# Optimization experiments

Measured on AMD Instinct MI355X. Metric: run time of the kernel, lower is better.

The kernel has to match this reference:

```python
import jax, jax.numpy as jnp
import numpy as np

VOCAB, DIM, B, S = 32000, 1024, 64, 512

def setup_inputs() -> dict:
    key = jax.random.key(0)
    ks = jax.random.split(key, 16)
    std = 1.0 / np.sqrt(DIM)
    return {
        "x": jax.random.randint(ks[0], (B,), 0, VOCAB),
        "h": jax.random.normal(ks[1], (B, DIM), jnp.float32),
        "c": jax.random.normal(ks[2], (B, DIM), jnp.float32),
        "enc_y": jax.random.normal(ks[3], (B, S, DIM), jnp.float32),
        "F_emb": jax.random.normal(ks[4], (VOCAB, DIM), jnp.float32),
        "W1_w": jax.random.uniform(ks[5], (DIM, DIM), jnp.float32, -std, std),
        "W1_b": jnp.zeros((DIM,), jnp.float32),
        "W2_w": jax.random.uniform(ks[6], (DIM, DIM), jnp.float32, -std, std),
        "W2_b": jnp.zeros((DIM,), jnp.float32),
        "V_w": jax.random.uniform(ks[7], (1, DIM), jnp.float32, -std, std),
        "V_b": jnp.zeros((1,), jnp.float32),
        "W_ih": jax.random.uniform(ks[8], (4 * DIM, DIM), jnp.float32, -std, std),
        "W_hh": jax.random.uniform(ks[9], (4 * DIM, DIM), jnp.float32, -std, std),
        "b_ih": jax.random.uniform(ks[10], (4 * DIM,), jnp.float32, -std, std),
        "b_hh": jax.random.uniform(ks[11], (4 * DIM,), jnp.float32, -std, std),
        "fc_w": jax.random.uniform(ks[12], (VOCAB, DIM), jnp.float32, -std, std),
        "fc_b": jnp.zeros((VOCAB,), jnp.float32),
    }

def reference(x, h, c, enc_y, F_emb, W1_w, W1_b, W2_w, W2_b, V_w, V_b,
              W_ih, W_hh, b_ih, b_hh, fc_w, fc_b):
    # Bahdanau additive attention (weights returned; context is dead code for layer=1)
    i_s = jnp.einsum('bsd,ed->bse', enc_y, W1_w) + W1_b          # [B,S,D]
    j_s = (h @ W2_w.T + W2_b)[:, None, :]                        # [B,1,D]
    score = jnp.tanh(i_s + j_s)                                  # [B,S,D]
    att = jax.nn.softmax(score @ V_w.T + V_b, axis=1)            # [B,S,1]
    # embedding lookup for the step token
    emb = F_emb[x]                                               # [B,D]
    # single-step LSTM (pytorch gate order: i, f, g, o)
    gates = emb @ W_ih.T + b_ih + h @ W_hh.T + b_hh              # [B,4D]
    ig, fg, gg, og = jnp.split(gates, 4, axis=-1)
    c_new = jax.nn.sigmoid(fg) * c + jax.nn.sigmoid(ig) * jnp.tanh(gg)
    h_new = jax.nn.sigmoid(og) * jnp.tanh(c_new)
    out = h_new + emb                                            # residual skip
    logits = out @ fc_w.T + fc_b                                 # [B,VOCAB]
    return logits, h_new, c_new, att
```

## Files before the change

kernel.cpp:

```cpp
#include <hip/hip_runtime.h>

#define DEV __device__ __forceinline__

typedef __bf16 bf16_t;
typedef bf16_t bf16x8 __attribute__((ext_vector_type(8)));
typedef float f32x4 __attribute__((ext_vector_type(4)));

static constexpr int VOCAB = 32000, DIM = 1024, BATCH = 64, SEQ = 512;
static constexpr int M_SC = BATCH * SEQ;

DEV unsigned short f2bf(float f) {
  unsigned u = __builtin_bit_cast(unsigned, f);
  u += 0x7FFFu + ((u >> 16) & 1u);
  return (unsigned short)(u >> 16);
}

DEV float sigmf(float x) {
  x = fminf(fmaxf(x, -30.f), 30.f);
  return 1.0f / (1.0f + __expf(-x));
}

DEV float tanh_fast(float x) {
  x = fminf(fmaxf(x, -20.f), 20.f);
  float e = __expf(2.0f * x);
  return (e - 1.0f) / (e + 1.0f);
}

DEV void gload_lds16(const void* g, void* l) {
  __builtin_amdgcn_global_load_lds(
      (__attribute__((address_space(1))) void*)(g),
      (__attribute__((address_space(3))) void*)(l), 16, 0, 0);
}

__global__ void __launch_bounds__(256) k_prep(const float* __restrict__ enc,
                                              const float* __restrict__ w1,
                                              unsigned short* __restrict__ enc_b,
                                              unsigned short* __restrict__ w1_b,
                                              float* __restrict__ att_l) {
  int gid = blockIdx.x * 256 + threadIdx.x;
  if (gid < M_SC) att_l[gid] = 0.f;
  const int ENC4 = (M_SC * DIM) / 4;
  const int TOT4 = ENC4 + (DIM * DIM) / 4;
  int stride = gridDim.x * 256;
  for (int i = gid; i < TOT4; i += stride) {
    float4 v;
    unsigned short* dst;
    if (i < ENC4) {
      v = ((const float4*)enc)[i];
      dst = enc_b + (size_t)i * 4;
    } else {
      v = ((const float4*)w1)[i - ENC4];
      dst = w1_b + (size_t)(i - ENC4) * 4;
    }
    ushort4 o;
    o.x = f2bf(v.x); o.y = f2bf(v.y); o.z = f2bf(v.z); o.w = f2bf(v.w);
    *(ushort4*)dst = o;
  }
}

__global__ void k_embed(const int* __restrict__ x, const float* __restrict__ Femb,
                        const float* __restrict__ h, float* __restrict__ emb_f,
                        unsigned short* __restrict__ eh_b, unsigned short* __restrict__ h_b) {
  int b = blockIdx.x;
  int tok = x[b];
  for (int d = threadIdx.x; d < DIM; d += blockDim.x) {
    float e = Femb[(size_t)tok * DIM + d];
    float hv = h[b * DIM + d];
    emb_f[b * DIM + d] = e;
    unsigned short eb = f2bf(e), hb = f2bf(hv);
    eh_b[b * 2 * DIM + d] = eb;
    eh_b[b * 2 * DIM + DIM + d] = hb;
    h_b[b * DIM + d] = hb;
  }
}

__global__ void __launch_bounds__(256) k_skinny(
    const unsigned short* __restrict__ A, int lda,
    const float* __restrict__ B1, const float* __restrict__ B2, int ksplit,
    const float* __restrict__ bias, float* __restrict__ C, int N, int K) {
  __shared__ unsigned short As[64 * 128];
  __shared__ unsigned short Bs[16 * 128];
  int t = threadIdx.x;
  int l = t & 63, w = t >> 6;
  int n0 = blockIdx.x * 16;
  f32x4 acc = {};
  int rx = (l & 7) << 3;

  for (int kt = 0; kt < K; kt += 128) {
    const float* Bsrc;
    int kk;
    if (kt < ksplit) { Bsrc = B1; kk = kt; } else { Bsrc = B2; kk = kt - ksplit; }
#pragma unroll
    for (int i = 0; i < 4; ++i) {
      int sbase = i * 256 + w * 64;
      int s = sbase + l;
      int row = s >> 4;
      int scol = ((s & 15) ^ (row & 7)) * 8;
      gload_lds16(A + (size_t)row * lda + kt + scol, &As[sbase * 8]);
    }
#pragma unroll
    for (int i = 0; i < 2; ++i) {
      int lin = i * 256 + t;
      int row = lin >> 5;
      int c4 = (lin & 31) * 4;
      float4 v = *(const float4*)(Bsrc + (size_t)(n0 + row) * 1024 + kk + c4);
      ushort4 o;
      o.x = f2bf(v.x); o.y = f2bf(v.y); o.z = f2bf(v.z); o.w = f2bf(v.w);
      *(ushort4*)&Bs[row * 128 + (c4 ^ ((row & 7) << 3))] = o;
    }
    __syncthreads();
#pragma unroll
    for (int kf = 0; kf < 4; ++kf) {
      int ko = kf * 32 + 8 * (l >> 4);
      int ar = w * 16 + (l & 15);
      bf16x8 af = *(const bf16x8*)&As[ar * 128 + (ko ^ rx)];
      bf16x8 bf = *(const bf16x8*)&Bs[(l & 15) * 128 + (ko ^ rx)];
      acc = __builtin_amdgcn_mfma_f32_16x16x32_bf16(af, bf, acc, 0, 0, 0);
    }
    __syncthreads();
  }
  int cn = n0 + (l & 15);
  float bv = bias ? bias[cn] : 0.f;
#pragma unroll
  for (int r = 0; r < 4; ++r) {
    int m = w * 16 + (l >> 4) * 4 + r;
    C[(size_t)m * N + cn] = acc[r] + bv;
  }
}

__global__ void __launch_bounds__(256) k_score(
    const unsigned short* __restrict__ encb, const unsigned short* __restrict__ w1mat,
    const float* __restrict__ js, const float* __restrict__ w1bias,
    const float* __restrict__ vw, float* __restrict__ att_l) {
  __shared__ unsigned short As[128 * 64];
  __shared__ unsigned short Bs[128 * 64];
  int t = threadIdx.x;
  int l = t & 63, w = t >> 6;
  int wr = w >> 1, wc = w & 1;
  int wg = blockIdx.x;
  int swz = (wg & 7) * 256 + (wg >> 3);
  int m0 = (swz >> 3) * 128;
  int n0 = (swz & 7) * 128;
  f32x4 acc[4][4] = {};

  int srow = l >> 3;
  int scol = ((l & 7) ^ (l >> 3)) * 8;
  int rx = (l & 7) << 3;

  for (int kt = 0; kt < 16; ++kt) {
    int kbase = kt * 64;
#pragma unroll
    for (int i = 0; i < 4; ++i) {
      int chunk = i * 4 + w;
      int row = chunk * 8 + srow;
      gload_lds16(encb + (size_t)(m0 + row) * DIM + kbase + scol, &As[chunk * 512]);
      gload_lds16(w1mat + (size_t)(n0 + row) * DIM + kbase + scol, &Bs[chunk * 512]);
    }
    __syncthreads();
#pragma unroll
    for (int kh = 0; kh < 2; ++kh) {
      int ko = kh * 32 + 8 * (l >> 4);
      int kos = ko ^ rx;
      bf16x8 bfr[4], afr[4];
#pragma unroll
      for (int ni = 0; ni < 4; ++ni)
        bfr[ni] = *(const bf16x8*)&Bs[(wc * 64 + ni * 16 + (l & 15)) * 64 + kos];
#pragma unroll
      for (int mi = 0; mi < 4; ++mi)
        afr[mi] = *(const bf16x8*)&As[(wr * 64 + mi * 16 + (l & 15)) * 64 + kos];
#pragma unroll
      for (int mi = 0; mi < 4; ++mi)
#pragma unroll
        for (int ni = 0; ni < 4; ++ni)
          acc[mi][ni] = __builtin_amdgcn_mfma_f32_16x16x32_bf16(afr[mi], bfr[ni], acc[mi][ni], 0, 0, 0);
    }
    __syncthreads();
  }

  int b = m0 >> 9;
  const float* jrow = js + b * DIM;
  float psum[4][4] = {};
#pragma unroll
  for (int ni = 0; ni < 4; ++ni) {
    int e = n0 + wc * 64 + ni * 16 + (l & 15);
    float jv = jrow[e] + w1bias[e];
    float vv = vw[e];
#pragma unroll
    for (int mi = 0; mi < 4; ++mi)
#pragma unroll
      for (int r = 0; r < 4; ++r)
        psum[mi][r] += tanh_fast(acc[mi][ni][r] + jv) * vv;
  }
#pragma unroll
  for (int mi = 0; mi < 4; ++mi)
#pragma unroll
    for (int r = 0; r < 4; ++r) {
      float s = psum[mi][r];
      s += __shfl_xor(s, 1);
      s += __shfl_xor(s, 2);
      s += __shfl_xor(s, 4);
      s += __shfl_xor(s, 8);
      if ((l & 15) == 0)
        atomicAdd(&att_l[m0 + wr * 64 + mi * 16 + (l >> 4) * 4 + r], s);
    }
}

__global__ void k_softmax(const float* __restrict__ att_l, float* __restrict__ att) {
  __shared__ float red[16];
  int b = blockIdx.x, t = threadIdx.x;
  float v = att_l[b * SEQ + t];
  float m = v;
#pragma unroll
  for (int o = 32; o; o >>= 1) m = fmaxf(m, __shfl_xor(m, o));
  if ((t & 63) == 0) red[t >> 6] = m;
  __syncthreads();
  m = red[0];
#pragma unroll
  for (int i = 1; i < 8; ++i) m = fmaxf(m, red[i]);
  float e = __expf(v - m);
  float s = e;
#pragma unroll
  for (int o = 32; o; o >>= 1) s += __shfl_xor(s, o);
  __syncthreads();
  if ((t & 63) == 0) red[8 + (t >> 6)] = s;
  __syncthreads();
  s = 0.f;
#pragma unroll
  for (int i = 0; i < 8; ++i) s += red[8 + i];
  att[b * SEQ + t] = e / s;
}

__global__ void k_lstm(const float* __restrict__ gates, const float* __restrict__ bih,
                       const float* __restrict__ bhh, const float* __restrict__ c,
                       const float* __restrict__ emb_f, float* __restrict__ out_h,
                       float* __restrict__ out_c, unsigned short* __restrict__ out_b) {
  int t = blockIdx.x * 256 + threadIdx.x;
  int b = t >> 10, d = t & 1023;
  const float* g = gates + b * 4 * DIM;
  float ig = g[d] + bih[d] + bhh[d];
  float fg = g[DIM + d] + bih[DIM + d] + bhh[DIM + d];
  float gg = g[2 * DIM + d] + bih[2 * DIM + d] + bhh[2 * DIM + d];
  float og = g[3 * DIM + d] + bih[3 * DIM + d] + bhh[3 * DIM + d];
  float cn = sigmf(fg) * c[t] + sigmf(ig) * tanh_fast(gg);
  float hn = sigmf(og) * tanh_fast(cn);
  out_h[t] = hn;
  out_c[t] = cn;
  out_b[t] = f2bf(hn + emb_f[t]);
}

extern "C" void kernel_launch(void* const* d_in, const int* in_sizes, int n_in,
                              void* d_out, int out_size, void* d_ws, size_t ws_size,
                              hipStream_t stream) {
  const int* x = (const int*)d_in[0];
  const float* h = (const float*)d_in[1];
  const float* c = (const float*)d_in[2];
  const float* enc = (const float*)d_in[3];
  const float* Femb = (const float*)d_in[4];
  const float* W1w = (const float*)d_in[5];
  const float* W1b = (const float*)d_in[6];
  const float* W2w = (const float*)d_in[7];
  const float* W2b = (const float*)d_in[8];
  const float* Vw = (const float*)d_in[9];
  const float* Wih = (const float*)d_in[11];
  const float* Whh = (const float*)d_in[12];
  const float* bih = (const float*)d_in[13];
  const float* bhh = (const float*)d_in[14];
  const float* fcw = (const float*)d_in[15];
  const float* fcb = (const float*)d_in[16];

  float* out_logits = (float*)d_out;
  float* out_h = out_logits + (size_t)BATCH * VOCAB;
  float* out_c = out_h + BATCH * DIM;
  float* out_att = out_c + BATCH * DIM;

  char* p = (char*)d_ws;
  unsigned short* enc_b = (unsigned short*)p; p += (size_t)M_SC * DIM * 2;
  unsigned short* w1_b = (unsigned short*)p;  p += (size_t)DIM * DIM * 2;
  float* att_l = (float*)p;                   p += (size_t)M_SC * 4;
  float* js = (float*)p;                      p += (size_t)BATCH * DIM * 4;
  float* emb_f = (float*)p;                   p += (size_t)BATCH * DIM * 4;
  unsigned short* eh_b = (unsigned short*)p;  p += (size_t)BATCH * 2 * DIM * 2;
  unsigned short* h_b = (unsigned short*)p;   p += (size_t)BATCH * DIM * 2;
  float* gates = (float*)p;                   p += (size_t)BATCH * 4 * DIM * 4;
  unsigned short* out_b = (unsigned short*)p; p += (size_t)BATCH * DIM * 2;

  hipLaunchKernelGGL(k_prep, dim3(2048), dim3(256), 0, stream, enc, W1w, enc_b, w1_b, att_l);
  hipLaunchKernelGGL(k_embed, dim3(BATCH), dim3(256), 0, stream, x, Femb, h, emb_f, eh_b, h_b);
  hipLaunchKernelGGL(k_skinny, dim3(DIM / 16), dim3(256), 0, stream,
                     h_b, DIM, W2w, W2w, DIM, W2b, js, DIM, DIM);
  hipLaunchKernelGGL(k_score, dim3(2048), dim3(256), 0, stream,
                     enc_b, w1_b, js, W1b, Vw, att_l);
  hipLaunchKernelGGL(k_softmax, dim3(BATCH), dim3(SEQ), 0, stream, att_l, out_att);
  hipLaunchKernelGGL(k_skinny, dim3(4 * DIM / 16), dim3(256), 0, stream,
                     eh_b, 2 * DIM, Wih, Whh, DIM, (const float*)nullptr, gates, 4 * DIM, 2 * DIM);
  hipLaunchKernelGGL(k_lstm, dim3(BATCH * DIM / 256), dim3(256), 0, stream,
                     gates, bih, bhh, c, emb_f, out_h, out_c, out_b);
  hipLaunchKernelGGL(k_skinny, dim3(VOCAB / 16), dim3(256), 0, stream,
                     out_b, DIM, fcw, fcw, DIM, fcb, out_logits, VOCAB, DIM);
}
```

Before: 211.2 us.

## Double-buffer LDS tiles in skinny GEMM and score GEMM kernels

Both the skinny GEMM and the attention-score GEMM now use two LDS buffers. The next K-tile is prefetched (direct global-to-LDS loads for A and the score operands, register-held float loads for the skinny B) while MFMAs run on the current tile, leaving one barrier per iteration instead of two. The aim is to hide global load latency behind compute. The cost is doubled LDS use, 64KB in k_score, which may lower occupancy, and a possible hazard: async LDS writes into the other buffer with no explicit vmcnt wait before the barrier.

```diff
diff --git a/kernel.cpp b/kernel.cpp
--- a/kernel.cpp
+++ b/kernel.cpp
@@ -78,47 +78,76 @@
     const unsigned short* __restrict__ A, int lda,
     const float* __restrict__ B1, const float* __restrict__ B2, int ksplit,
     const float* __restrict__ bias, float* __restrict__ C, int N, int K) {
-  __shared__ unsigned short As[64 * 128];
-  __shared__ unsigned short Bs[16 * 128];
+  __shared__ unsigned short As[2][64 * 128];
+  __shared__ unsigned short Bs[2][16 * 128];
   int t = threadIdx.x;
   int l = t & 63, w = t >> 6;
   int n0 = blockIdx.x * 16;
   f32x4 acc = {};
   int rx = (l & 7) << 3;
 
-  for (int kt = 0; kt < K; kt += 128) {
+  int brow = 0, bc4 = 0;
+  float4 vB[2];
+
+  auto loadB = [&](int k0) {
     const float* Bsrc;
     int kk;
-    if (kt < ksplit) { Bsrc = B1; kk = kt; } else { Bsrc = B2; kk = kt - ksplit; }
+    if (k0 < ksplit) { Bsrc = B1; kk = k0; } else { Bsrc = B2; kk = k0 - ksplit; }
+#pragma unroll
+    for (int i = 0; i < 2; ++i) {
+      int lin = i * 256 + t;
+      int row = lin >> 5, c4 = (lin & 31) * 4;
+      vB[i] = *(const float4*)(Bsrc + (size_t)(n0 + row) * 1024 + kk + c4);
+    }
+  };
+  auto writeB = [&](int bufi) {
+#pragma unroll
+    for (int i = 0; i < 2; ++i) {
+      int lin = i * 256 + t;
+      int row = lin >> 5, c4 = (lin & 31) * 4;
+      ushort4 o;
+      o.x = f2bf(vB[i].x); o.y = f2bf(vB[i].y); o.z = f2bf(vB[i].z); o.w = f2bf(vB[i].w);
+      *(ushort4*)&Bs[bufi][row * 128 + (c4 ^ ((row & 7) << 3))] = o;
+    }
+  };
+  auto stageA = [&](int k0, int bufi) {
 #pragma unroll
     for (int i = 0; i < 4; ++i) {
       int sbase = i * 256 + w * 64;
       int s = sbase + l;
       int row = s >> 4;
       int scol = ((s & 15) ^ (row & 7)) * 8;
-      gload_lds16(A + (size_t)row * lda + kt + scol, &As[sbase * 8]);
-    }
-#pragma unroll
-    for (int i = 0; i < 2; ++i) {
-      int lin = i * 256 + t;
-      int row = lin >> 5;
-      int c4 = (lin & 31) * 4;
-      float4 v = *(const float4*)(Bsrc + (size_t)(n0 + row) * 1024 + kk + c4);
-      ushort4 o;
-      o.x = f2bf(v.x); o.y = f2bf(v.y); o.z = f2bf(v.z); o.w = f2bf(v.w);
-      *(ushort4*)&Bs[row * 128 + (c4 ^ ((row & 7) << 3))] = o;
-    }
-    __syncthreads();
+      gload_lds16(A + (size_t)row * lda + k0 + scol, &As[bufi][sbase * 8]);
+    }
+  };
+
+  loadB(0);
+  stageA(0, 0);
+  writeB(0);
+  __syncthreads();
+
+  int nk = K / 128;
+  int cur = 0;
+  for (int kt = 0; kt < nk; ++kt) {
+    bool pref = (kt + 1 < nk);
+    if (pref) {
+      loadB((kt + 1) * 128);
+      stageA((kt + 1) * 128, cur ^ 1);
+    }
 #pragma unroll
     for (int kf = 0; kf < 4; ++kf) {
       int ko = kf * 32 + 8 * (l >> 4);
       int ar = w * 16 + (l & 15);
-      bf16x8 af = *(const bf16x8*)&As[ar * 128 + (ko ^ rx)];
-      bf16x8 bf = *(const bf16x8*)&Bs[(l & 15) * 128 + (ko ^ rx)];
+      bf16x8 af = *(const bf16x8*)&As[cur][ar * 128 + (ko ^ rx)];
+      bf16x8 bf = *(const bf16x8*)&Bs[cur][(l & 15) * 128 + (ko ^ rx)];
       acc = __builtin_amdgcn_mfma_f32_16x16x32_bf16(af, bf, acc, 0, 0, 0);
     }
+    if (pref) writeB(cur ^ 1);
     __syncthreads();
-  }
+    cur ^= 1;
+  }
+  (void)brow; (void)bc4;
+
   int cn = n0 + (l & 15);
   float bv = bias ? bias[cn] : 0.f;
 #pragma unroll
@@ -132,8 +161,8 @@
     const unsigned short* __restrict__ encb, const unsigned short* __restrict__ w1mat,
     const float* __restrict__ js, const float* __restrict__ w1bias,
     const float* __restrict__ vw, float* __restrict__ att_l) {
-  __shared__ unsigned short As[128 * 64];
-  __shared__ unsigned short Bs[128 * 64];
+  __shared__ unsigned short As[2][128 * 64];
+  __shared__ unsigned short Bs[2][128 * 64];
   int t = threadIdx.x;
   int l = t & 63, w = t >> 6;
   int wr = w >> 1, wc = w & 1;
@@ -147,16 +176,26 @@
   int scol = ((l & 7) ^ (l >> 3)) * 8;
   int rx = (l & 7) << 3;
 
-  for (int kt = 0; kt < 16; ++kt) {
+  const unsigned short* pa = encb + (size_t)m0 * DIM;
+  const unsigned short* pb = w1mat + (size_t)n0 * DIM;
+
+  auto stage = [&](int kt, int bufi) {
     int kbase = kt * 64;
 #pragma unroll
     for (int i = 0; i < 4; ++i) {
       int chunk = i * 4 + w;
       int row = chunk * 8 + srow;
-      gload_lds16(encb + (size_t)(m0 + row) * DIM + kbase + scol, &As[chunk * 512]);
-      gload_lds16(w1mat + (size_t)(n0 + row) * DIM + kbase + scol, &Bs[chunk * 512]);
-    }
-    __syncthreads();
+      gload_lds16(pa + (size_t)row * DIM + kbase + scol, &As[bufi][chunk * 512]);
+      gload_lds16(pb + (size_t)row * DIM + kbase + scol, &Bs[bufi][chunk * 512]);
+    }
+  };
+
+  stage(0, 0);
+  __syncthreads();
+
+  int cur = 0;
+  for (int kt = 0; kt < 16; ++kt) {
+    if (kt < 15) stage(kt + 1, cur ^ 1);
 #pragma unroll
     for (int kh = 0; kh < 2; ++kh) {
       int ko = kh * 32 + 8 * (l >> 4);
@@ -164,10 +203,10 @@
       bf16x8 bfr[4], afr[4];
 #pragma unroll
       for (int ni = 0; ni < 4; ++ni)
-        bfr[ni] = *(const bf16x8*)&Bs[(wc * 64 + ni * 16 + (l & 15)) * 64 + kos];
+        bfr[ni] = *(const bf16x8*)&Bs[cur][(wc * 64 + ni * 16 + (l & 15)) * 64 + kos];
 #pragma unroll
       for (int mi = 0; mi < 4; ++mi)
-        afr[mi] = *(const bf16x8*)&As[(wr * 64 + mi * 16 + (l & 15)) * 64 + kos];
+        afr[mi] = *(const bf16x8*)&As[cur][(wr * 64 + mi * 16 + (l & 15)) * 64 + kos];
 #pragma unroll
       for (int mi = 0; mi < 4; ++mi)
 #pragma unroll
@@ -175,6 +214,7 @@
           acc[mi][ni] = __builtin_amdgcn_mfma_f32_16x16x32_bf16(afr[mi], bfr[ni], acc[mi][ni], 0, 0, 0);
     }
     __syncthreads();
+    cur ^= 1;
   }
 
   int b = m0 >> 9;
```

After: 215.9 us. 2.2% more time.
